# Kernel tuning notes

Hardware: AMD Instinct MI355X
Metric: run time of the kernel (lower is better)

The kernel has to match this reference:

```python
import jax, jax.numpy as jnp
import numpy as np

B, S, D, H = 4, 2048, 512, 8
DEPTH = D // H
BAND = 16  # log_thresholds [1,2,4,8,16] union == distance <= 16


def setup_inputs() -> dict:
    key = jax.random.key(0)
    ks = jax.random.split(key, 11)
    sc = 0.02
    return {
        "q": jax.random.normal(ks[0], (B, S, D), jnp.float32),
        "k": jax.random.normal(ks[1], (B, S, D), jnp.float32),
        "v": jax.random.normal(ks[2], (B, S, D), jnp.float32),
        "wq": jax.random.normal(ks[3], (D, D), jnp.float32) * sc,
        "bq": jnp.zeros((D,), jnp.float32),
        "wk": jax.random.normal(ks[4], (D, D), jnp.float32) * sc,
        "bk": jnp.zeros((D,), jnp.float32),
        "wv": jax.random.normal(ks[5], (D, D), jnp.float32) * sc,
        "bv": jnp.zeros((D,), jnp.float32),
        "wo": jax.random.normal(ks[6], (D, D), jnp.float32) * sc,
        "bo": jnp.zeros((D,), jnp.float32),
    }


def _split_heads(x):
    # [B,S,D] -> [B,H,S,depth]
    b, s, _ = x.shape
    return x.reshape(b, s, H, DEPTH).transpose(0, 2, 1, 3)


def reference(q, k, v, wq, bq, wk, bk, wv, bv, wo, bo):
    qh = _split_heads(q @ wq + bq)
    kh = _split_heads(k @ wk + bk)
    vh = _split_heads(v @ wv + bv)
    scale = 1.0 / jnp.sqrt(jnp.float32(DEPTH))
    logits = jnp.einsum("bhqd,bhkd->bhqk", qh, kh) * scale  # [B,H,S,S]
    idx = jnp.arange(S)
    keep = jnp.abs(idx[:, None] - idx[None, :]) <= BAND  # band mask [S,S]
    logits = jnp.where(keep[None, None], logits, jnp.float32(-1e9))
    attn = jax.nn.softmax(logits, axis=-1)
    out = jnp.einsum("bhqk,bhkd->bhqd", attn, vh)
    out = out.transpose(0, 2, 1, 3).reshape(q.shape[0], -1, D)
    return out @ wo + bo
```

## Files before the change

kernel.cpp:

```cpp
#include <hip/hip_runtime.h>

typedef unsigned int uint;
typedef unsigned short ushort;
typedef __attribute__((ext_vector_type(8))) short bf16x8;
typedef __attribute__((ext_vector_type(4))) float f32x4;

namespace {
constexpr int kS = 2048;
constexpr int kD = 512;
constexpr int kH = 8;
constexpr int kNT = 8192;
constexpr int kBand = 16;
}

static __device__ __forceinline__ ushort f2bf(float f) {
  uint u = __builtin_bit_cast(uint, f);
  u = (u + 0x7fffu + ((u >> 16) & 1u)) >> 16;
  return (ushort)u;
}

#define GLD16(gp, lp)                                                   \
  __builtin_amdgcn_global_load_lds(                                     \
      (const __attribute__((address_space(1))) uint*)(gp),              \
      (__attribute__((address_space(3))) uint*)(lp), 16, 0, 0)

__global__ __launch_bounds__(256) void prep_w_kernel(
    const float* __restrict__ wq, const float* __restrict__ wk,
    const float* __restrict__ wv, const float* __restrict__ wo,
    ushort* __restrict__ WT) {
  const float* W;
  switch (blockIdx.z) {
    case 0: W = wq; break;
    case 1: W = wk; break;
    case 2: W = wv; break;
    default: W = wo; break;
  }
  ushort* T = WT + (size_t)blockIdx.z * kD * kD;
  __shared__ float Ws[64][65];
  const int tid = threadIdx.x;
  const int kt = blockIdx.x * 64, nt = blockIdx.y * 64;
  const int r = tid >> 2, c0 = (tid & 3) * 16;
#pragma unroll
  for (int i = 0; i < 4; ++i) {
    const float4 x = *(const float4*)(W + (size_t)(kt + r) * kD + nt + c0 + i * 4);
    Ws[r][c0 + i * 4 + 0] = x.x;
    Ws[r][c0 + i * 4 + 1] = x.y;
    Ws[r][c0 + i * 4 + 2] = x.z;
    Ws[r][c0 + i * 4 + 3] = x.w;
  }
  __syncthreads();
  const int n = tid >> 2, k0 = (tid & 3) * 16;
  alignas(16) ushort tmp[16];
#pragma unroll
  for (int i = 0; i < 16; ++i) tmp[i] = f2bf(Ws[k0 + i][n]);
  ushort* dst = T + (size_t)(nt + n) * kD + kt + k0;
  *(uint4*)(dst + 0) = *(const uint4*)&tmp[0];
  *(uint4*)(dst + 8) = *(const uint4*)&tmp[8];
}

__global__ __launch_bounds__(256) void prep_act_kernel(
    const float* __restrict__ q, const float* __restrict__ k,
    ushort* __restrict__ qb, ushort* __restrict__ kb) {
  const float* src = blockIdx.y ? k : q;
  ushort* dst = blockIdx.y ? kb : qb;
  const size_t i8 = ((size_t)blockIdx.x * 256 + threadIdx.x) * 8;
  const float4 x0 = *(const float4*)(src + i8);
  const float4 x1 = *(const float4*)(src + i8 + 4);
  alignas(16) ushort t8[8] = {f2bf(x0.x), f2bf(x0.y), f2bf(x0.z), f2bf(x0.w),
                              f2bf(x1.x), f2bf(x1.y), f2bf(x1.z), f2bf(x1.w)};
  *(uint4*)(dst + i8) = *(const uint4*)t8;
}

__global__ __launch_bounds__(256) void gemm_kernel(
    const ushort* __restrict__ qb, const ushort* __restrict__ kb,
    const float* __restrict__ vf, const ushort* __restrict__ obp,
    const ushort* __restrict__ WT, const float* __restrict__ bq,
    const float* __restrict__ bk, const float* __restrict__ bv,
    const float* __restrict__ bo, ushort* __restrict__ Qp,
    ushort* __restrict__ Kp, ushort* __restrict__ VT,
    float* __restrict__ outp, int mode_arg) {
  const int mode = mode_arg + blockIdx.z;
  const ushort* Ab = nullptr;
  const float* Af = nullptr;
  const float* bias;
  switch (mode) {
    case 0: Ab = qb; bias = bq; break;
    case 1: Ab = kb; bias = bk; break;
    case 2: Af = vf; bias = bv; break;
    default: Ab = obp; bias = bo; break;
  }
  const ushort* BT = WT + (size_t)mode * kD * kD;

  __shared__ alignas(16) ushort Asm[128 * 32];
  __shared__ alignas(16) ushort Bsm[128 * 32];

  const int tid = threadIdx.x;
  const int wave = tid >> 6, lane = tid & 63, l15 = lane & 15, qd = lane >> 4;
  const int wm = (wave >> 1) * 64, wn = (wave & 1) * 64;
  const int row0 = blockIdx.y * 128, col0 = blockIdx.x * 128;
  const int sw = (l15 & 3) ^ (l15 >> 2);

  int lr[2], lg[2];
#pragma unroll
  for (int i = 0; i < 2; ++i) {
    const int linear = i * 256 + tid;
    lr[i] = linear >> 2;
    const int c = linear & 3;
    lg[i] = c ^ ((lr[i] & 3) ^ ((lr[i] >> 2) & 3));
  }

  f32x4 acc[4][4];
#pragma unroll
  for (int mi = 0; mi < 4; ++mi)
#pragma unroll
    for (int ni = 0; ni < 4; ++ni) acc[mi][ni] = (f32x4)(0.f);

  for (int k0 = 0; k0 < kD; k0 += 32) {
    if (mode == 2) {
#pragma unroll
      for (int i = 0; i < 2; ++i) {
        const float* ap = Af + (size_t)(row0 + lr[i]) * kD + k0 + lg[i] * 8;
        const float4 x0 = *(const float4*)ap;
        const float4 x1 = *(const float4*)(ap + 4);
        alignas(16) ushort t8[8] = {f2bf(x0.x), f2bf(x0.y), f2bf(x0.z),
                                    f2bf(x0.w), f2bf(x1.x), f2bf(x1.y),
                                    f2bf(x1.z), f2bf(x1.w)};
        *(uint4*)&Asm[(i * 256 + tid) * 8] = *(const uint4*)t8;
      }
    } else {
#pragma unroll
      for (int i = 0; i < 2; ++i)
        GLD16(Ab + (size_t)(row0 + lr[i]) * kD + k0 + lg[i] * 8,
              &Asm[(i * 256 + wave * 64) * 8]);
    }
#pragma unroll
    for (int i = 0; i < 2; ++i)
      GLD16(BT + (size_t)(col0 + lr[i]) * kD + k0 + lg[i] * 8,
            &Bsm[(i * 256 + wave * 64) * 8]);
    __syncthreads();

    bf16x8 af[4], br[4];
#pragma unroll
    for (int mi = 0; mi < 4; ++mi)
      af[mi] = *(const bf16x8*)&Asm[(wm + mi * 16 + l15) * 32 + (qd ^ sw) * 8];
#pragma unroll
    for (int ni = 0; ni < 4; ++ni)
      br[ni] = *(const bf16x8*)&Bsm[(wn + ni * 16 + l15) * 32 + (qd ^ sw) * 8];
#pragma unroll
    for (int mi = 0; mi < 4; ++mi)
#pragma unroll
      for (int ni = 0; ni < 4; ++ni)
        acc[mi][ni] = __builtin_amdgcn_mfma_f32_16x16x32_bf16(
            af[mi], br[ni], acc[mi][ni], 0, 0, 0);
    __syncthreads();
  }

  float bcol[4];
#pragma unroll
  for (int ni = 0; ni < 4; ++ni) bcol[ni] = bias[col0 + wn + ni * 16 + l15];

  if (mode <= 1) {
    ushort* C = (mode == 0) ? Qp : Kp;
#pragma unroll
    for (int mi = 0; mi < 4; ++mi)
#pragma unroll
      for (int ni = 0; ni < 4; ++ni) {
        const int n_g = col0 + wn + ni * 16 + l15;
#pragma unroll
        for (int r = 0; r < 4; ++r) {
          const int token = row0 + wm + mi * 16 + qd * 4 + r;
          C[(size_t)token * kD + n_g] = f2bf(acc[mi][ni][r] + bcol[ni]);
        }
      }
  } else if (mode == 2) {
#pragma unroll
    for (int mi = 0; mi < 4; ++mi)
#pragma unroll
      for (int ni = 0; ni < 4; ++ni) {
        const int n_g = col0 + wn + ni * 16 + l15;
        const int h = n_g >> 6, d = n_g & 63;
        const int t0 = row0 + wm + mi * 16 + qd * 4;
        const int b = t0 >> 11, ss = t0 & (kS - 1);
        alignas(8) ushort t4[4];
#pragma unroll
        for (int r = 0; r < 4; ++r) t4[r] = f2bf(acc[mi][ni][r] + bcol[ni]);
        *(uint2*)&VT[((size_t)(b * kH + h) * 64 + d) * kS + ss] =
            *(const uint2*)t4;
      }
  } else {
#pragma unroll
    for (int mi = 0; mi < 4; ++mi)
#pragma unroll
      for (int ni = 0; ni < 4; ++ni) {
        const int n_g = col0 + wn + ni * 16 + l15;
#pragma unroll
        for (int r = 0; r < 4; ++r) {
          const int token = row0 + wm + mi * 16 + qd * 4 + r;
          outp[(size_t)token * kD + n_g] = acc[mi][ni][r] + bcol[ni];
        }
      }
  }
}

__global__ __launch_bounds__(64, 1) void attn_kernel(
    const ushort* __restrict__ Qp, const ushort* __restrict__ Kp,
    const ushort* __restrict__ VT, ushort* __restrict__ Ob) {
  __shared__ alignas(16) ushort Pl[64 * 104];

  const int lane = threadIdx.x, l15 = lane & 15, qd = lane >> 4;
  const int bh = blockIdx.y, b = bh >> 3, h = bh & 7;
  const int q0 = blockIdx.x * 64;
  const int colA = h * 64;

  bf16x8 qf[4][2], kf[6][2];
#pragma unroll
  for (int mi = 0; mi < 4; ++mi) {
    const size_t base =
        ((size_t)b * kS + q0 + mi * 16 + l15) * kD + colA + qd * 8;
#pragma unroll
    for (int kc = 0; kc < 2; ++kc)
      qf[mi][kc] = *(const bf16x8*)&Qp[base + kc * 32];
  }
#pragma unroll
  for (int ni = 0; ni < 6; ++ni) {
    int key = q0 - kBand + ni * 16 + l15;
    key = key < 0 ? 0 : (key > kS - 1 ? kS - 1 : key);
    const size_t base = ((size_t)b * kS + key) * kD + colA + qd * 8;
#pragma unroll
    for (int kc = 0; kc < 2; ++kc)
      kf[ni][kc] = *(const bf16x8*)&Kp[base + kc * 32];
  }

  f32x4 S[4][6];
#pragma unroll
  for (int mi = 0; mi < 4; ++mi)
#pragma unroll
    for (int ni = 0; ni < 6; ++ni) S[mi][ni] = (f32x4)(0.f);
#pragma unroll
  for (int mi = 0; mi < 4; ++mi)
#pragma unroll
    for (int ni = 0; ni < 6; ++ni)
#pragma unroll
      for (int kc = 0; kc < 2; ++kc)
        S[mi][ni] = __builtin_amdgcn_mfma_f32_16x16x32_bf16(
            qf[mi][kc], kf[ni][kc], S[mi][ni], 0, 0, 0);

#pragma unroll
  for (int mi = 0; mi < 4; ++mi)
#pragma unroll
    for (int ni = 0; ni < 6; ++ni)
#pragma unroll
      for (int r = 0; r < 4; ++r) {
        const int q_local = mi * 16 + qd * 4 + r;
        const int key_local = ni * 16 + l15;
        const int key = q0 - kBand + key_local;
        const int dlt = key_local - q_local;
        const bool ok = (dlt >= 0) && (dlt <= 32) && (key >= 0) && (key < kS);
        S[mi][ni][r] = ok ? S[mi][ni][r] * 0.125f : -3.0e38f;
      }

  float inv[4][4];
#pragma unroll
  for (int mi = 0; mi < 4; ++mi)
#pragma unroll
    for (int r = 0; r < 4; ++r) {
      float m = S[mi][0][r];
#pragma unroll
      for (int ni = 1; ni < 6; ++ni) m = fmaxf(m, S[mi][ni][r]);
      m = fmaxf(m, __shfl_xor(m, 1));
      m = fmaxf(m, __shfl_xor(m, 2));
      m = fmaxf(m, __shfl_xor(m, 4));
      m = fmaxf(m, __shfl_xor(m, 8));
      float s = 0.f;
#pragma unroll
      for (int ni = 0; ni < 6; ++ni) {
        const float e = __expf(S[mi][ni][r] - m);
        S[mi][ni][r] = e;
        s += e;
      }
      s += __shfl_xor(s, 1);
      s += __shfl_xor(s, 2);
      s += __shfl_xor(s, 4);
      s += __shfl_xor(s, 8);
      inv[mi][r] = 1.f / s;
    }

#pragma unroll
  for (int mi = 0; mi < 4; ++mi)
#pragma unroll
    for (int ni = 0; ni < 6; ++ni)
#pragma unroll
      for (int r = 0; r < 4; ++r)
        Pl[(mi * 16 + qd * 4 + r) * 104 + ni * 16 + l15] = f2bf(S[mi][ni][r]);
  __syncthreads();

  f32x4 O[4][4];
#pragma unroll
  for (int mi = 0; mi < 4; ++mi)
#pragma unroll
    for (int nt = 0; nt < 4; ++nt) O[mi][nt] = (f32x4)(0.f);

#pragma unroll
  for (int kc = 0; kc < 3; ++kc) {
    bf16x8 pf[4], vfr[4];
#pragma unroll
    for (int mi = 0; mi < 4; ++mi)
      pf[mi] = *(const bf16x8*)&Pl[(mi * 16 + l15) * 104 + kc * 32 + qd * 8];
    int kb0 = q0 - kBand + kc * 32 + qd * 8;
    kb0 = kb0 < 0 ? 0 : (kb0 > kS - 8 ? kS - 8 : kb0);
#pragma unroll
    for (int nt = 0; nt < 4; ++nt)
      vfr[nt] = *(const bf16x8*)&VT[((size_t)bh * 64 + nt * 16 + l15) * kS + kb0];
#pragma unroll
    for (int mi = 0; mi < 4; ++mi)
#pragma unroll
      for (int nt = 0; nt < 4; ++nt)
        O[mi][nt] = __builtin_amdgcn_mfma_f32_16x16x32_bf16(pf[mi], vfr[nt],
                                                            O[mi][nt], 0, 0, 0);
  }

#pragma unroll
  for (int mi = 0; mi < 4; ++mi)
#pragma unroll
    for (int nt = 0; nt < 4; ++nt)
#pragma unroll
      for (int r = 0; r < 4; ++r) {
        const int tok = b * kS + q0 + mi * 16 + qd * 4 + r;
        Ob[(size_t)tok * kD + colA + nt * 16 + l15] =
            f2bf(O[mi][nt][r] * inv[mi][r]);
      }
}

extern "C" void kernel_launch(void* const* d_in, const int* in_sizes, int n_in,
                              void* d_out, int out_size, void* d_ws,
                              size_t ws_size, hipStream_t stream) {
  const float* q = (const float*)d_in[0];
  const float* k = (const float*)d_in[1];
  const float* v = (const float*)d_in[2];
  const float* wq = (const float*)d_in[3];
  const float* bq = (const float*)d_in[4];
  const float* wk = (const float*)d_in[5];
  const float* bk = (const float*)d_in[6];
  const float* wv = (const float*)d_in[7];
  const float* bv = (const float*)d_in[8];
  const float* wo = (const float*)d_in[9];
  const float* bo = (const float*)d_in[10];
  float* out = (float*)d_out;

  ushort* qb = (ushort*)d_ws;
  ushort* kb = qb + (size_t)kNT * kD;
  ushort* Qp = kb + (size_t)kNT * kD;
  ushort* Kp = Qp + (size_t)kNT * kD;
  ushort* VT = Kp + (size_t)kNT * kD;
  ushort* WT = VT + (size_t)kNT * kD;
  ushort* Ob = qb;

  prep_w_kernel<<<dim3(8, 8, 4), 256, 0, stream>>>(wq, wk, wv, wo, WT);
  prep_act_kernel<<<dim3(2048, 2), 256, 0, stream>>>(q, k, qb, kb);
  gemm_kernel<<<dim3(4, 64, 3), 256, 0, stream>>>(
      qb, kb, v, Ob, WT, bq, bk, bv, bo, Qp, Kp, VT, out, 0);
  attn_kernel<<<dim3(kS / 64, 32), 64, 0, stream>>>(Qp, Kp, VT, Ob);
  gemm_kernel<<<dim3(4, 64, 1), 256, 0, stream>>>(
      qb, kb, v, Ob, WT, bq, bk, bv, bo, Qp, Kp, VT, out, 3);
}
```

Baseline: 180.9 us.

## Merge prep kernels, triple-buffer GEMM loads, and stage epilogue stores through LDS

```diff
diff --git a/kernel.cpp b/kernel.cpp
--- a/kernel.cpp
+++ b/kernel.cpp
@@ -24,25 +24,38 @@
       (const __attribute__((address_space(1))) uint*)(gp),              \
       (__attribute__((address_space(3))) uint*)(lp), 16, 0, 0)
 
-__global__ __launch_bounds__(256) void prep_w_kernel(
-    const float* __restrict__ wq, const float* __restrict__ wk,
-    const float* __restrict__ wv, const float* __restrict__ wo,
+__global__ __launch_bounds__(256) void prep_kernel(
+    const float* __restrict__ q, const float* __restrict__ k,
+    const float* __restrict__ v, const float* __restrict__ wq,
+    const float* __restrict__ wk, const float* __restrict__ wv,
+    const float* __restrict__ wo, ushort* __restrict__ qb,
+    ushort* __restrict__ kb, ushort* __restrict__ vb,
     ushort* __restrict__ WT) {
-  const float* W;
-  switch (blockIdx.z) {
-    case 0: W = wq; break;
-    case 1: W = wk; break;
-    case 2: W = wv; break;
-    default: W = wo; break;
-  }
-  ushort* T = WT + (size_t)blockIdx.z * kD * kD;
   __shared__ float Ws[64][65];
+  const int blk = blockIdx.x;
   const int tid = threadIdx.x;
-  const int kt = blockIdx.x * 64, nt = blockIdx.y * 64;
+  if (blk < 6144) {
+    const int z = blk >> 11, t = blk & 2047;
+    const float* src = z == 0 ? q : (z == 1 ? k : v);
+    ushort* dst = z == 0 ? qb : (z == 1 ? kb : vb);
+    const size_t i8 = ((size_t)t * 256 + tid) * 8;
+    const float4 x0 = *(const float4*)(src + i8);
+    const float4 x1 = *(const float4*)(src + i8 + 4);
+    alignas(16) ushort t8[8] = {f2bf(x0.x), f2bf(x0.y), f2bf(x0.z), f2bf(x0.w),
+                                f2bf(x1.x), f2bf(x1.y), f2bf(x1.z), f2bf(x1.w)};
+    *(uint4*)(dst + i8) = *(const uint4*)t8;
+    return;
+  }
+  const int w = blk - 6144;
+  const int z = w >> 6;
+  const float* W = z == 0 ? wq : (z == 1 ? wk : (z == 2 ? wv : wo));
+  ushort* T = WT + (size_t)z * kD * kD;
+  const int kt = ((w >> 3) & 7) * 64, nt = (w & 7) * 64;
   const int r = tid >> 2, c0 = (tid & 3) * 16;
 #pragma unroll
   for (int i = 0; i < 4; ++i) {
-    const float4 x = *(const float4*)(W + (size_t)(kt + r) * kD + nt + c0 + i * 4);
+    const float4 x =
+        *(const float4*)(W + (size_t)(kt + r) * kD + nt + c0 + i * 4);
     Ws[r][c0 + i * 4 + 0] = x.x;
     Ws[r][c0 + i * 4 + 1] = x.y;
     Ws[r][c0 + i * 4 + 2] = x.z;
@@ -58,41 +71,26 @@
   *(uint4*)(dst + 8) = *(const uint4*)&tmp[8];
 }
 
-__global__ __launch_bounds__(256) void prep_act_kernel(
-    const float* __restrict__ q, const float* __restrict__ k,
-    ushort* __restrict__ qb, ushort* __restrict__ kb) {
-  const float* src = blockIdx.y ? k : q;
-  ushort* dst = blockIdx.y ? kb : qb;
-  const size_t i8 = ((size_t)blockIdx.x * 256 + threadIdx.x) * 8;
-  const float4 x0 = *(const float4*)(src + i8);
-  const float4 x1 = *(const float4*)(src + i8 + 4);
-  alignas(16) ushort t8[8] = {f2bf(x0.x), f2bf(x0.y), f2bf(x0.z), f2bf(x0.w),
-                              f2bf(x1.x), f2bf(x1.y), f2bf(x1.z), f2bf(x1.w)};
-  *(uint4*)(dst + i8) = *(const uint4*)t8;
-}
-
 __global__ __launch_bounds__(256) void gemm_kernel(
     const ushort* __restrict__ qb, const ushort* __restrict__ kb,
-    const float* __restrict__ vf, const ushort* __restrict__ obp,
+    const ushort* __restrict__ vb, const ushort* __restrict__ obp,
     const ushort* __restrict__ WT, const float* __restrict__ bq,
     const float* __restrict__ bk, const float* __restrict__ bv,
     const float* __restrict__ bo, ushort* __restrict__ Qp,
     ushort* __restrict__ Kp, ushort* __restrict__ VT,
     float* __restrict__ outp, int mode_arg) {
   const int mode = mode_arg + blockIdx.z;
-  const ushort* Ab = nullptr;
-  const float* Af = nullptr;
+  const ushort* Ab;
   const float* bias;
   switch (mode) {
     case 0: Ab = qb; bias = bq; break;
     case 1: Ab = kb; bias = bk; break;
-    case 2: Af = vf; bias = bv; break;
+    case 2: Ab = vb; bias = bv; break;
     default: Ab = obp; bias = bo; break;
   }
   const ushort* BT = WT + (size_t)mode * kD * kD;
 
-  __shared__ alignas(16) ushort Asm[128 * 32];
-  __shared__ alignas(16) ushort Bsm[128 * 32];
+  __shared__ alignas(16) ushort smem[24576];
 
   const int tid = threadIdx.x;
   const int wave = tid >> 6, lane = tid & 63, l15 = lane & 15, qd = lane >> 4;
@@ -100,13 +98,26 @@
   const int row0 = blockIdx.y * 128, col0 = blockIdx.x * 128;
   const int sw = (l15 & 3) ^ (l15 >> 2);
 
-  int lr[2], lg[2];
+  const ushort* pA[2];
+  const ushort* pB[2];
+  uint ldsA[2], ldsB[2];
 #pragma unroll
   for (int i = 0; i < 2; ++i) {
     const int linear = i * 256 + tid;
-    lr[i] = linear >> 2;
-    const int c = linear & 3;
-    lg[i] = c ^ ((lr[i] & 3) ^ ((lr[i] >> 2) & 3));
+    const int r = linear >> 2, c = linear & 3;
+    const int g = c ^ ((r & 3) ^ ((r >> 2) & 3));
+    pA[i] = Ab + (size_t)(row0 + r) * kD + g * 8;
+    pB[i] = BT + (size_t)(col0 + r) * kD + g * 8;
+    ldsA[i] = (uint)(i * 256 + wave * 64) * 8;
+    ldsB[i] = 12288u + (uint)(i * 256 + wave * 64) * 8;
+  }
+
+#define ISSUE(kk, st)                                  \
+  {                                                    \
+    GLD16(pA[0] + (kk), &smem[ldsA[0] + (st) * 4096]); \
+    GLD16(pA[1] + (kk), &smem[ldsA[1] + (st) * 4096]); \
+    GLD16(pB[0] + (kk), &smem[ldsB[0] + (st) * 4096]); \
+    GLD16(pB[1] + (kk), &smem[ldsB[1] + (st) * 4096]); \
   }
 
   f32x4 acc[4][4];
@@ -115,79 +126,40 @@
 #pragma unroll
     for (int ni = 0; ni < 4; ++ni) acc[mi][ni] = (f32x4)(0.f);
 
-  for (int k0 = 0; k0 < kD; k0 += 32) {
-    if (mode == 2) {
-#pragma unroll
-      for (int i = 0; i < 2; ++i) {
-        const float* ap = Af + (size_t)(row0 + lr[i]) * kD + k0 + lg[i] * 8;
-        const float4 x0 = *(const float4*)ap;
-        const float4 x1 = *(const float4*)(ap + 4);
-        alignas(16) ushort t8[8] = {f2bf(x0.x), f2bf(x0.y), f2bf(x0.z),
-                                    f2bf(x0.w), f2bf(x1.x), f2bf(x1.y),
-                                    f2bf(x1.z), f2bf(x1.w)};
-        *(uint4*)&Asm[(i * 256 + tid) * 8] = *(const uint4*)t8;
-      }
-    } else {
-#pragma unroll
-      for (int i = 0; i < 2; ++i)
-        GLD16(Ab + (size_t)(row0 + lr[i]) * kD + k0 + lg[i] * 8,
-              &Asm[(i * 256 + wave * 64) * 8]);
-    }
-#pragma unroll
-    for (int i = 0; i < 2; ++i)
-      GLD16(BT + (size_t)(col0 + lr[i]) * kD + k0 + lg[i] * 8,
-            &Bsm[(i * 256 + wave * 64) * 8]);
-    __syncthreads();
-
+  ISSUE(0, 0);
+  ISSUE(32, 1);
+#pragma unroll
+  for (int it = 0; it < 16; ++it) {
+    if (it < 15)
+      asm volatile("s_waitcnt vmcnt(4) lgkmcnt(0)\n\ts_barrier" ::: "memory");
+    else
+      asm volatile("s_waitcnt vmcnt(0) lgkmcnt(0)\n\ts_barrier" ::: "memory");
+    if (it < 14) ISSUE((it + 2) * 32, (it + 2) % 3);
+    const ushort* as = &smem[(it % 3) * 4096];
+    const ushort* bs = &smem[12288 + (it % 3) * 4096];
     bf16x8 af[4], br[4];
 #pragma unroll
     for (int mi = 0; mi < 4; ++mi)
-      af[mi] = *(const bf16x8*)&Asm[(wm + mi * 16 + l15) * 32 + (qd ^ sw) * 8];
+      af[mi] = *(const bf16x8*)&as[(wm + mi * 16 + l15) * 32 + (qd ^ sw) * 8];
 #pragma unroll
     for (int ni = 0; ni < 4; ++ni)
-      br[ni] = *(const bf16x8*)&Bsm[(wn + ni * 16 + l15) * 32 + (qd ^ sw) * 8];
+      br[ni] = *(const bf16x8*)&bs[(wn + ni * 16 + l15) * 32 + (qd ^ sw) * 8];
 #pragma unroll
     for (int mi = 0; mi < 4; ++mi)
 #pragma unroll
       for (int ni = 0; ni < 4; ++ni)
         acc[mi][ni] = __builtin_amdgcn_mfma_f32_16x16x32_bf16(
             af[mi], br[ni], acc[mi][ni], 0, 0, 0);
-    __syncthreads();
-  }
+  }
+#undef ISSUE
+
+  __syncthreads();
 
   float bcol[4];
 #pragma unroll
   for (int ni = 0; ni < 4; ++ni) bcol[ni] = bias[col0 + wn + ni * 16 + l15];
 
-  if (mode <= 1) {
-    ushort* C = (mode == 0) ? Qp : Kp;
-#pragma unroll
-    for (int mi = 0; mi < 4; ++mi)
-#pragma unroll
-      for (int ni = 0; ni < 4; ++ni) {
-        const int n_g = col0 + wn + ni * 16 + l15;
-#pragma unroll
-        for (int r = 0; r < 4; ++r) {
-          const int token = row0 + wm + mi * 16 + qd * 4 + r;
-          C[(size_t)token * kD + n_g] = f2bf(acc[mi][ni][r] + bcol[ni]);
-        }
-      }
-  } else if (mode == 2) {
-#pragma unroll
-    for (int mi = 0; mi < 4; ++mi)
-#pragma unroll
-      for (int ni = 0; ni < 4; ++ni) {
-        const int n_g = col0 + wn + ni * 16 + l15;
-        const int h = n_g >> 6, d = n_g & 63;
-        const int t0 = row0 + wm + mi * 16 + qd * 4;
-        const int b = t0 >> 11, ss = t0 & (kS - 1);
-        alignas(8) ushort t4[4];
-#pragma unroll
-        for (int r = 0; r < 4; ++r) t4[r] = f2bf(acc[mi][ni][r] + bcol[ni]);
-        *(uint2*)&VT[((size_t)(b * kH + h) * 64 + d) * kS + ss] =
-            *(const uint2*)t4;
-      }
-  } else {
+  if (mode == 3) {
 #pragma unroll
     for (int mi = 0; mi < 4; ++mi)
 #pragma unroll
@@ -199,6 +171,47 @@
           outp[(size_t)token * kD + n_g] = acc[mi][ni][r] + bcol[ni];
         }
       }
+    return;
+  }
+
+  ushort* T = &smem[wave * 4608];
+  if (mode <= 1) {
+#pragma unroll
+    for (int mi = 0; mi < 4; ++mi)
+#pragma unroll
+      for (int ni = 0; ni < 4; ++ni)
+#pragma unroll
+        for (int r = 0; r < 4; ++r)
+          T[(mi * 16 + qd * 4 + r) * 72 + ni * 16 + l15] =
+              f2bf(acc[mi][ni][r] + bcol[ni]);
+  } else {
+#pragma unroll
+    for (int mi = 0; mi < 4; ++mi)
+#pragma unroll
+      for (int ni = 0; ni < 4; ++ni)
+#pragma unroll
+        for (int r = 0; r < 4; ++r)
+          T[(ni * 16 + l15) * 72 + mi * 16 + qd * 4 + r] =
+              f2bf(acc[mi][ni][r] + bcol[ni]);
+  }
+  asm volatile("s_waitcnt lgkmcnt(0)" ::: "memory");
+
+  const ushort* Trow = &smem[wave * 4608 + lane * 72];
+  if (mode <= 1) {
+    ushort* C = (mode == 0) ? Qp : Kp;
+    ushort* dst = C + (size_t)(row0 + wm + lane) * kD + col0 + wn;
+#pragma unroll
+    for (int c = 0; c < 8; ++c)
+      *(uint4*)(dst + c * 8) = *(const uint4*)(Trow + c * 8);
+  } else {
+    const int n_g = col0 + wn + lane;
+    const int h = n_g >> 6, d = n_g & 63;
+    const int t0 = row0 + wm;
+    const int b = t0 >> 11, ss = t0 & (kS - 1);
+    ushort* dst = VT + ((size_t)(b * kH + h) * 64 + d) * kS + ss;
+#pragma unroll
+    for (int c = 0; c < 8; ++c)
+      *(uint4*)(dst + c * 8) = *(const uint4*)(Trow + c * 8);
   }
 }
 
@@ -310,7 +323,8 @@
     kb0 = kb0 < 0 ? 0 : (kb0 > kS - 8 ? kS - 8 : kb0);
 #pragma unroll
     for (int nt = 0; nt < 4; ++nt)
-      vfr[nt] = *(const bf16x8*)&VT[((size_t)bh * 64 + nt * 16 + l15) * kS + kb0];
+      vfr[nt] =
+          *(const bf16x8*)&VT[((size_t)bh * 64 + nt * 16 + l15) * kS + kb0];
 #pragma unroll
     for (int mi = 0; mi < 4; ++mi)
 #pragma unroll
@@ -324,11 +338,16 @@
 #pragma unroll
     for (int nt = 0; nt < 4; ++nt)
 #pragma unroll
-      for (int r = 0; r < 4; ++r) {
-        const int tok = b * kS + q0 + mi * 16 + qd * 4 + r;
-        Ob[(size_t)tok * kD + colA + nt * 16 + l15] =
+      for (int r = 0; r < 4; ++r)
+        Pl[(mi * 16 + qd * 4 + r) * 72 + nt * 16 + l15] =
             f2bf(O[mi][nt][r] * inv[mi][r]);
-      }
+  asm volatile("s_waitcnt lgkmcnt(0)" ::: "memory");
+
+  ushort* dst = Ob + ((size_t)b * kS + q0 + lane) * kD + colA;
+  const ushort* Trow = &Pl[lane * 72];
+#pragma unroll
+  for (int c = 0; c < 8; ++c)
+    *(uint4*)(dst + c * 8) = *(const uint4*)(Trow + c * 8);
 }
 
 extern "C" void kernel_launch(void* const* d_in, const int* in_sizes, int n_in,
@@ -349,17 +368,20 @@
 
   ushort* qb = (ushort*)d_ws;
   ushort* kb = qb + (size_t)kNT * kD;
-  ushort* Qp = kb + (size_t)kNT * kD;
-  ushort* Kp = Qp + (size_t)kNT * kD;
+  ushort* vb = kb + (size_t)kNT * kD;
+  ushort* Kp = vb + (size_t)kNT * kD;
   ushort* VT = Kp + (size_t)kNT * kD;
   ushort* WT = VT + (size_t)kNT * kD;
-  ushort* Ob = qb;
-
-  prep_w_kernel<<<dim3(8, 8, 4), 256, 0, stream>>>(wq, wk, wv, wo, WT);
-  prep_act_kernel<<<dim3(2048, 2), 256, 0, stream>>>(q, k, qb, kb);
-  gemm_kernel<<<dim3(4, 64, 3), 256, 0, stream>>>(
-      qb, kb, v, Ob, WT, bq, bk, bv, bo, Qp, Kp, VT, out, 0);
+  ushort* Qp = vb;
+  ushort* Ob = kb;
+
+  prep_kernel<<<dim3(6400), 256, 0, stream>>>(q, k, v, wq, wk, wv, wo, qb, kb,
+                                              vb, WT);
+  gemm_kernel<<<dim3(4, 64, 2), 256, 0, stream>>>(
+      qb, kb, vb, Ob, WT, bq, bk, bv, bo, Qp, Kp, VT, out, 1);
+  gemm_kernel<<<dim3(4, 64, 1), 256, 0, stream>>>(
+      qb, kb, vb, Ob, WT, bq, bk, bv, bo, Qp, Kp, VT, out, 0);
   attn_kernel<<<dim3(kS / 64, 32), 64, 0, stream>>>(Qp, Kp, VT, Ob);
   gemm_kernel<<<dim3(4, 64, 1), 256, 0, stream>>>(
-      qb, kb, v, Ob, WT, bq, bk, bv, bo, Qp, Kp, VT, out, 3);
-}
+      qb, kb, vb, Ob, WT, bq, bk, bv, bo, Qp, Kp, VT, out, 3);
+}
```

Result: faster. 170.3 us (-5.9%).
